# Kernel optimization log

Hardware: AMD Instinct MI355X
Metric: run time of the kernel (lower is better)

Reference implementation:

```python
import jax, jax.numpy as jnp
import numpy as np

B, S, D, H = 2, 2048, 1024, 16
DH = D // H  # d_head = 64
EPS = 1e-6


def _rms_norm(x, eps=EPS):
    # norm_without_weight: RMS normalization over last dim, no learned scale
    return x * jax.lax.rsqrt(jnp.mean(x * x, axis=-1, keepdims=True) + eps)


def _rope_tables(seq_len, dim):
    # angular_freq: dim//4 geometric freqs + dim//4 zeros -> dim//2 total
    freqs = (1.0 / 1024.0) ** jnp.linspace(0.0, 1.0, dim // 4, dtype=jnp.float32)
    freqs = jnp.concatenate([freqs, jnp.zeros((dim // 4,), dtype=jnp.float32)])
    theta = jnp.outer(jnp.arange(seq_len, dtype=jnp.float32), freqs)  # [S, dim//2]
    return jnp.cos(theta), jnp.sin(theta)


def _apply_rope(x_bhsk, cos, sin):
    # x: [B,H,S,DH]; cos/sin: [S, DH//2] broadcast over batch/heads
    c = cos[None, None, :, :]
    s = sin[None, None, :, :]
    xf = x_bhsk.astype(jnp.float32)
    x1, x2 = jnp.split(xf, 2, axis=-1)
    y1 = x1 * c + x2 * s
    y2 = -x1 * s + x2 * c
    return jnp.concatenate([y1, y2], axis=-1).astype(x_bhsk.dtype)


def setup_inputs() -> dict:
    key = jax.random.key(0)
    k0, k1, k2, k3, k4 = jax.random.split(key, 5)
    scale = 1.0 / np.sqrt(D)
    x = jax.random.normal(k0, (B, S, D), dtype=jnp.float32)
    # equinox Linear stores weight as [out_features, in_features], y = x @ W.T
    w_q = jax.random.normal(k1, (D, D), dtype=jnp.float32) * scale
    w_k = jax.random.normal(k2, (D, D), dtype=jnp.float32) * scale
    w_v = jax.random.normal(k3, (D, D), dtype=jnp.float32) * scale
    w_o = jax.random.normal(k4, (D, D), dtype=jnp.float32) * scale
    mask = jnp.tril(jnp.ones((S, S), dtype=bool))  # causal
    return {"x": x, "w_q": w_q, "w_k": w_k, "w_v": w_v, "w_o": w_o, "mask": mask}


def reference(x, w_q, w_k, w_v, w_o, mask):
    b, s, d = x.shape
    # projections (no bias); [B,S,D] @ [D,D].T -> [B,S,D] -> [B,H,S,DH]
    def proj(w):
        y = jnp.einsum('bsd,ed->bse', x, w)
        return y.reshape(b, s, H, DH).transpose(0, 2, 1, 3)
    q, k, v = proj(w_q), proj(w_k), proj(w_v)
    # QK-norm (RMS, no weight)
    q = _rms_norm(q)
    k = _rms_norm(k)
    # rotary over sequence axis
    cos, sin = _rope_tables(s, DH)
    q = _apply_rope(q, cos, sin)
    k = _apply_rope(k, cos, sin)
    # scores [B,H,S,S]
    scores = jnp.einsum('bhsk,bhtk->bhst', q, k) / jnp.sqrt(jnp.float32(DH))
    scores = jnp.where(mask[None, None, :, :], scores, -jnp.inf)
    weights = jax.nn.softmax(scores, axis=-1)
    out = jnp.einsum('bhst,bhtk->bhsk', weights, v)  # [B,H,S,DH]
    out = out.transpose(0, 2, 1, 3).reshape(b, s, d)
    return jnp.einsum('bsd,ed->bse', out, w_o)
```

## Files before the change

kernel.cpp:

```cpp
#include <hip/hip_runtime.h>
#include <hip/hip_bf16.h>

#define Bb 2
#define Ss 2048
#define Dd 1024
#define Hh 16
#define Tt ((size_t)Bb*Ss*Dd)
#define WNn ((size_t)Dd*Dd)

typedef short bf16x8 __attribute__((ext_vector_type(8)));
typedef short bf16x4 __attribute__((ext_vector_type(4)));
typedef float floatx4 __attribute__((ext_vector_type(4)));
typedef unsigned short u16;

__device__ inline void gld16(void* lds, const void* g) {
  __builtin_amdgcn_global_load_lds(
      (const __attribute__((address_space(1))) unsigned int*)g,
      (__attribute__((address_space(3))) unsigned int*)lds, 16, 0, 0);
}

__device__ inline float bf2f(u16 u) {
  unsigned int x = ((unsigned int)u) << 16;
  float f; __builtin_memcpy(&f, &x, 4); return f;
}
__device__ inline u16 f2bf(float f) {
  unsigned int x; __builtin_memcpy(&x, &f, 4);
  x = (x + 0x7fff + ((x >> 16) & 1)) >> 16;
  return (u16)x;
}
__device__ inline float u2f(unsigned int x) {
  float f; __builtin_memcpy(&f, &x, 4); return f;
}
__device__ inline unsigned int cvtpk(float lo, float hi) {
  unsigned int r;
  asm("v_cvt_pk_bf16_f32 %0, %1, %2" : "=v"(r) : "v"(lo), "v"(hi));
  return r;
}

__global__ void sniff(const unsigned int* __restrict__ x, unsigned int* __restrict__ flag,
                      int nwords) {
  __shared__ int cnt;
  if (threadIdx.x == 0) cnt = 0;
  __syncthreads();
  int local = 0;
  for (int i = threadIdx.x; i < nwords; i += blockDim.x) {
    unsigned int wd = x[i];
    if (((wd >> 7)  & 0xFFu) == 0xFFu) local++;
    if (((wd >> 23) & 0xFFu) == 0xFFu) local++;
  }
  atomicAdd(&cnt, local);
  __syncthreads();
  if (threadIdx.x == 0) *flag = (cnt >= 64) ? 1u : 0u;
}

__global__ __launch_bounds__(256) void convert_all(
    const void* __restrict__ x,  const void* __restrict__ wq,
    const void* __restrict__ wk, const void* __restrict__ wv,
    const void* __restrict__ wo, u16* __restrict__ dst,
    int smode, const unsigned int* __restrict__ flag,
    float2* __restrict__ tab) {
  const int gb = blockIdx.x;
  if (gb >= 4096) {
    int e = (gb - 4096)*1024 + threadIdx.x*4;
#pragma unroll
    for (int j = 0; j < 4; j++, e++) {
      int s = e >> 4, f = e & 15;
      float freq = exp2f((-10.0f/15.0f) * (float)f);
      float th = (float)s * freq;
      float sn, c;
      sincosf(th, &sn, &c);
      tab[e] = make_float2(c, sn);
    }
    return;
  }
  const void* src; size_t base; int lb;
  if (gb < 2048)      { src = x;  base = 0;            lb = gb;        }
  else if (gb < 2560) { src = wq; base = Tt;           lb = gb - 2048; }
  else if (gb < 3072) { src = wk; base = Tt + WNn;     lb = gb - 2560; }
  else if (gb < 3584) { src = wv; base = Tt + 2*WNn;   lb = gb - 3072; }
  else                { src = wo; base = Tt + 3*WNn;   lb = gb - 3584; }
  const size_t off = (size_t)lb*2048 + threadIdx.x*8;
  const bool f32 = (smode >= 0) ? (smode == 1) : (*flag != 0u);
  bf16x8 v;
  if (f32) {
    const float* s = (const float*)src + off;
#pragma unroll
    for (int j = 0; j < 8; j++) v[j] = (short)f2bf(s[j]);
  } else {
    v = *(const bf16x8*)((const u16*)src + off);
  }
  *(bf16x8*)(dst + base + off) = v;
}

__global__ __launch_bounds__(256) void gemm_bt(
    const u16* __restrict__ A,
    const u16* __restrict__ W0, const u16* __restrict__ W1, const u16* __restrict__ W2,
    void* __restrict__ C0, void* __restrict__ C1, void* __restrict__ C2,
    int M, int N, int K, const float2* __restrict__ tab)
{
  const u16* W; void* C;
  if (blockIdx.z == 0)      { W = W0; C = C0; }
  else if (blockIdx.z == 1) { W = W1; C = C1; }
  else                      { W = W2; C = C2; }

  __shared__ __align__(16) u16 sA[128*32];
  __shared__ __align__(16) u16 sB[128*32];
  __shared__ __align__(16) u16 sE[4][64*72];

  const int tid  = threadIdx.x;
  const int lane = tid & 63;
  const int w    = tid >> 6;
  const int wm = w >> 1, wn = w & 1;
  const int col = lane & 15, quad = lane >> 4;
  const int bm = blockIdx.y, bn = blockIdx.x;

  floatx4 acc[4][4] = {};

  const int c0 = tid, c1 = tid + 256;
  const size_t aOff0 = (size_t)(bm*128 + (c0 >> 2))*K + (c0 & 3)*8;
  const size_t aOff1 = (size_t)(bm*128 + (c1 >> 2))*K + (c1 & 3)*8;
  const size_t bOff0 = (size_t)(bn*128 + (c0 >> 2))*K + (c0 & 3)*8;
  const size_t bOff1 = (size_t)(bn*128 + (c1 >> 2))*K + (c1 & 3)*8;

  for (int kk = 0; kk < K; kk += 32) {
    gld16(&sA[c0*8], A + aOff0 + kk);
    gld16(&sA[c1*8], A + aOff1 + kk);
    gld16(&sB[c0*8], W + bOff0 + kk);
    gld16(&sB[c1*8], W + bOff1 + kk);
    __syncthreads();
    bf16x8 af[4], bfr[4];
#pragma unroll
    for (int i = 0; i < 4; i++)
      af[i] = *(const bf16x8*)&sA[(wm*64 + i*16 + col)*32 + quad*8];
#pragma unroll
    for (int j = 0; j < 4; j++)
      bfr[j] = *(const bf16x8*)&sB[(wn*64 + j*16 + col)*32 + quad*8];
#pragma unroll
    for (int i = 0; i < 4; i++)
#pragma unroll
      for (int j = 0; j < 4; j++)
        acc[i][j] = __builtin_amdgcn_mfma_f32_16x16x32_bf16(af[i], bfr[j], acc[i][j], 0, 0, 0);
    __syncthreads();
  }

  u16* sEw = &sE[w][0];
  const int rrow = lane >> 3, rch = lane & 7;

  if (blockIdx.z == 2) {
#pragma unroll
    for (int i = 0; i < 4; i++)
#pragma unroll
      for (int j = 0; j < 4; j++) {
        bf16x4 pk;
#pragma unroll
        for (int r = 0; r < 4; r++) pk[r] = (short)f2bf(acc[i][j][r]);
        *(bf16x4*)&sEw[(j*16 + col)*72 + i*16 + quad*4] = pk;
      }
    const int g0 = bm*128 + wm*64;
    const int bb = g0 >> 11, s0 = g0 & (Ss - 1);
    const int hh = (bn*128 + wn*64) >> 6;
    u16* Ct = (u16*)C;
#pragma unroll
    for (int t = 0; t < 8; t++) {
      const int dl = rrow + t*8;
      bf16x8 v = *(const bf16x8*)&sEw[dl*72 + rch*8];
      *(bf16x8*)&Ct[((size_t)(bb*Hh + hh)*64 + dl)*Ss + s0 + rch*8] = v;
    }
  } else {
    const float qs = (blockIdx.z == 0) ? 0.125f : 1.0f;
#pragma unroll
    for (int i = 0; i < 4; i++)
#pragma unroll
      for (int r = 0; r < 4; r++) {
        float ss = 0.0f;
#pragma unroll
        for (int j = 0; j < 4; j++) ss += acc[i][j][r]*acc[i][j][r];
        ss += __shfl_xor(ss, 1, 64);
        ss += __shfl_xor(ss, 2, 64);
        ss += __shfl_xor(ss, 4, 64);
        ss += __shfl_xor(ss, 8, 64);
        float rn = rsqrtf(ss*(1.0f/64.0f) + 1e-6f) * qs;
        int grow = bm*128 + wm*64 + i*16 + quad*4 + r;
        float2 cs = tab[(grow & (Ss - 1))*16 + col];
        float x0 = acc[i][0][r]*rn, x1 = acc[i][1][r]*rn;
        float x2 = acc[i][2][r]*rn, x3 = acc[i][3][r]*rn;
        const int lr = (i*16 + quad*4 + r)*72;
        sEw[lr + col]      = f2bf(x0*cs.x + x2*cs.y);
        sEw[lr + 16 + col] = f2bf(x1);
        sEw[lr + 32 + col] = f2bf(x2*cs.x - x0*cs.y);
        sEw[lr + 48 + col] = f2bf(x3);
      }
    u16* Co = (u16*)C;
    const size_t gb = (size_t)(bm*128 + wm*64);
    const int cb = bn*128 + wn*64 + rch*8;
#pragma unroll
    for (int t = 0; t < 8; t++) {
      const int lr = rrow + t*8;
      bf16x8 v = *(const bf16x8*)&sEw[lr*72 + rch*8];
      *(bf16x8*)&Co[(gb + lr)*N + cb] = v;
    }
  }
}

__global__ __launch_bounds__(256) void gemm_o(
    const u16* __restrict__ A, const u16* __restrict__ W, void* __restrict__ C,
    int M, int N, int K, const unsigned int* __restrict__ flag, int outMode)
{
  __shared__ __align__(16) u16 sA[128*32];
  __shared__ __align__(16) u16 sB[64*32];

  const int tid  = threadIdx.x;
  const int lane = tid & 63;
  const int w    = tid >> 6;
  const int wm = w >> 1, wn = w & 1;
  const int col = lane & 15, quad = lane >> 4;
  const int bm = blockIdx.y, bn = blockIdx.x;

  floatx4 acc[4][2] = {};

  const int c0 = tid, c1 = tid + 256;
  const size_t aOff0 = (size_t)(bm*128 + (c0 >> 2))*K + (c0 & 3)*8;
  const size_t aOff1 = (size_t)(bm*128 + (c1 >> 2))*K + (c1 & 3)*8;
  const size_t bOff0 = (size_t)(bn*64  + (c0 >> 2))*K + (c0 & 3)*8;

  for (int kk = 0; kk < K; kk += 32) {
    gld16(&sA[c0*8], A + aOff0 + kk);
    gld16(&sA[c1*8], A + aOff1 + kk);
    gld16(&sB[c0*8], W + bOff0 + kk);
    __syncthreads();
    bf16x8 af[4], bfr[2];
#pragma unroll
    for (int i = 0; i < 4; i++)
      af[i] = *(const bf16x8*)&sA[(wm*64 + i*16 + col)*32 + quad*8];
#pragma unroll
    for (int j = 0; j < 2; j++)
      bfr[j] = *(const bf16x8*)&sB[(wn*32 + j*16 + col)*32 + quad*8];
#pragma unroll
    for (int i = 0; i < 4; i++)
#pragma unroll
      for (int j = 0; j < 2; j++)
        acc[i][j] = __builtin_amdgcn_mfma_f32_16x16x32_bf16(af[i], bfr[j], acc[i][j], 0, 0, 0);
    __syncthreads();
  }

  const bool f32o = (outMode == 1) || (outMode == -1 && *flag != 0u);
#pragma unroll
  for (int i = 0; i < 4; i++)
#pragma unroll
    for (int j = 0; j < 2; j++)
#pragma unroll
      for (int r = 0; r < 4; r++) {
        int grow = bm*128 + wm*64 + i*16 + quad*4 + r;
        int gcol = bn*64 + wn*32 + j*16 + col;
        size_t idx = (size_t)grow*N + gcol;
        float v = acc[i][j][r];
        if (f32o) ((float*)C)[idx] = v;
        else      ((u16*)C)[idx]   = f2bf(v);
      }
}

__global__ __launch_bounds__(256) void attn(
    const u16* __restrict__ Q, const u16* __restrict__ Kv,
    const u16* __restrict__ Vt, u16* __restrict__ O)
{
  __shared__ __align__(16) u16 sK[2][64*72];
  __shared__ __align__(16) u16 sV[2][2][64*32];
  __shared__ __align__(16) u16 sP[4][16*72];

  const int tid  = threadIdx.x;
  const int lane = tid & 63;
  const int w    = tid >> 6;
  const int col = lane & 15, quad = lane >> 4;
  const int bh = blockIdx.x;
  const int qt = 31 - (int)blockIdx.y;
  const int b = bh >> 4, h = bh & 15;
  const size_t base  = (size_t)b*Ss*Dd + (size_t)h*64;
  const size_t vbase = (size_t)bh*64*Ss;

  const int krow = tid >> 2;
  const int kch  = (tid & 3) * 2;
  const int vrow = tid >> 2;
  const int vcp  = (tid & 3) ^ (vrow & 3) ^ ((vrow >> 2) & 3);
  const u16* Vh = Vt + vbase + (size_t)vrow*Ss + vcp*8;
  const int xorv = quad ^ (col & 3) ^ ((col >> 2) & 3);
  u16* sPw = &sP[w][0];
  const float L2E = 1.44269504f;

  const int q0 = qt * 64;
  const int nk = qt + 1;
  const int qmin = q0 + w*16;

  bf16x8 qf0, qf1;
  {
    const size_t qoff = base + (size_t)(q0 + w*16 + col)*Dd + quad*8;
    qf0 = *(const bf16x8*)(Q + qoff);
    qf1 = *(const bf16x8*)(Q + qoff + 32);
  }
  floatx4 oacc[4] = {};
  float mi[4], li[4];
#pragma unroll
  for (int r = 0; r < 4; r++) { mi[r] = -1e30f; li[r] = 0.0f; }

  {
    const u16* kg = Kv + base + (size_t)krow*Dd + kch*8;
    bf16x8 ka = *(const bf16x8*)kg;
    bf16x8 kb = *(const bf16x8*)(kg + 8);
    gld16(&sV[0][0][tid*8], Vh);
    gld16(&sV[0][1][tid*8], Vh + 32);
    *(bf16x8*)&sK[0][krow*72 + kch*8]     = ka;
    *(bf16x8*)&sK[0][krow*72 + kch*8 + 8] = kb;
    __syncthreads();
  }

  for (int kt = 0; kt < nk; kt++) {
    const int t0 = kt*64;
    const int cur = kt & 1, nxt = cur ^ 1;
    const bool more = (kt + 1 < nk);
    bf16x8 ka, kb;
    if (more) {
      const u16* kg = Kv + base + (size_t)(t0 + 64 + krow)*Dd + kch*8;
      ka = *(const bf16x8*)kg;
      kb = *(const bf16x8*)(kg + 8);
      gld16(&sV[nxt][0][tid*8], Vh + t0 + 64);
      gld16(&sV[nxt][1][tid*8], Vh + t0 + 96);
    }

    floatx4 sc[4] = {};
    __builtin_amdgcn_s_setprio(1);
#pragma unroll
    for (int ts = 0; ts < 4; ts++) {
      bf16x8 k0 = *(const bf16x8*)&sK[cur][(ts*16 + col)*72 + quad*8];
      bf16x8 k1 = *(const bf16x8*)&sK[cur][(ts*16 + col)*72 + 32 + quad*8];
      sc[ts] = __builtin_amdgcn_mfma_f32_16x16x32_bf16(qf0, k0, sc[ts], 0,0,0);
      sc[ts] = __builtin_amdgcn_mfma_f32_16x16x32_bf16(qf1, k1, sc[ts], 0,0,0);
    }
    __builtin_amdgcn_s_setprio(0);

    const bool boundary = (t0 + 63 > qmin);
    float mxr[4];
    float needmax = 0.0f;
#pragma unroll
    for (int r = 0; r < 4; r++) {
      if (boundary) {
        const int qr = q0 + w*16 + quad*4 + r;
        if (t0 +      col > qr) sc[0][r] = -1e30f;
        if (t0 + 16 + col > qr) sc[1][r] = -1e30f;
        if (t0 + 32 + col > qr) sc[2][r] = -1e30f;
        if (t0 + 48 + col > qr) sc[3][r] = -1e30f;
      }
      float mx = fmaxf(fmaxf(sc[0][r], sc[1][r]), fmaxf(sc[2][r], sc[3][r]));
      mx = fmaxf(mx, __shfl_xor(mx, 1, 64));
      mx = fmaxf(mx, __shfl_xor(mx, 2, 64));
      mx = fmaxf(mx, __shfl_xor(mx, 4, 64));
      mx = fmaxf(mx, __shfl_xor(mx, 8, 64));
      mxr[r] = mx;
      needmax = fmaxf(needmax, mx - mi[r]);
    }
    if (!__all(needmax <= 8.0f)) {
      float alr[4];
#pragma unroll
      for (int r = 0; r < 4; r++) {
        float mn = fmaxf(mi[r], mxr[r]);
        float al = exp2f((mi[r] - mn)*L2E);
        mi[r] = mn; li[r] *= al; alr[r] = al;
      }
#pragma unroll
      for (int db = 0; db < 4; db++)
#pragma unroll
        for (int r = 0; r < 4; r++) oacc[db][r] *= alr[r];
    }
#pragma unroll
    for (int r = 0; r < 4; r++) {
      const float nb = -mi[r]*L2E;
      float p0 = exp2f(fmaf(sc[0][r], L2E, nb));
      float p1 = exp2f(fmaf(sc[1][r], L2E, nb));
      float p2 = exp2f(fmaf(sc[2][r], L2E, nb));
      float p3 = exp2f(fmaf(sc[3][r], L2E, nb));
      unsigned int pk01 = cvtpk(p0, p1);
      unsigned int pk23 = cvtpk(p2, p3);
      const int rw = (quad*4 + r)*72;
      sPw[rw + col]      = (u16)pk01;
      sPw[rw + 16 + col] = (u16)(pk01 >> 16);
      sPw[rw + 32 + col] = (u16)pk23;
      sPw[rw + 48 + col] = (u16)(pk23 >> 16);
      li[r] += (u2f(pk01 << 16) + u2f(pk01 & 0xffff0000u))
             + (u2f(pk23 << 16) + u2f(pk23 & 0xffff0000u));
    }
    bf16x8 pa0 = *(const bf16x8*)&sPw[col*72 + quad*8];
    bf16x8 pa1 = *(const bf16x8*)&sPw[col*72 + 32 + quad*8];
    __builtin_amdgcn_s_setprio(1);
#pragma unroll
    for (int db = 0; db < 4; db++) {
      const int vs = (db*16 + col)*32 + xorv*8;
      bf16x8 vb0 = *(const bf16x8*)&sV[cur][0][vs];
      bf16x8 vb1 = *(const bf16x8*)&sV[cur][1][vs];
      oacc[db] = __builtin_amdgcn_mfma_f32_16x16x32_bf16(pa0, vb0, oacc[db], 0,0,0);
      oacc[db] = __builtin_amdgcn_mfma_f32_16x16x32_bf16(pa1, vb1, oacc[db], 0,0,0);
    }
    __builtin_amdgcn_s_setprio(0);

    if (more) {
      *(bf16x8*)&sK[nxt][krow*72 + kch*8]     = ka;
      *(bf16x8*)&sK[nxt][krow*72 + kch*8 + 8] = kb;
    }
    __syncthreads();
  }

  float inv[4];
#pragma unroll
  for (int r = 0; r < 4; r++) {
    float s = li[r];
    s += __shfl_xor(s, 1, 64);
    s += __shfl_xor(s, 2, 64);
    s += __shfl_xor(s, 4, 64);
    s += __shfl_xor(s, 8, 64);
    inv[r] = 1.0f / s;
  }
#pragma unroll
  for (int db = 0; db < 4; db++)
#pragma unroll
    for (int r = 0; r < 4; r++)
      O[base + (size_t)(q0 + w*16 + quad*4 + r)*Dd + db*16 + col] =
          f2bf(oacc[db][r] * inv[r]);
}

extern "C" void kernel_launch(void* const* d_in, const int* in_sizes, int n_in,
                              void* d_out, int out_size, void* d_ws, size_t ws_size,
                              hipStream_t stream) {
  const void* x  = d_in[0];
  const void* wq = d_in[1];
  const void* wk = d_in[2];
  const void* wv = d_in[3];
  const void* wo = d_in[4];

  const size_t T  = Tt;
  const size_t WN = WNn;

  char* ws = (char*)d_ws;
  unsigned int* flag = (unsigned int*)ws;
  u16* xb  = (u16*)(ws + 256);
  u16* wqb = xb  + T;
  u16* wkb = wqb + WN;
  u16* wvb = wkb + WN;
  u16* wob = wvb + WN;
  u16* Qb  = wob + WN;
  u16* Kb  = Qb + T;
  u16* Vb  = Kb + T;
  u16* AO  = Vb + T;
  float2* tab = (float2*)(AO + T);

  int smode = -1;
  if (in_sizes && n_in > 0) {
    if (in_sizes[0] == (int)(T*4))      smode = 1;
    else if (in_sizes[0] == (int)(T*2)) smode = 0;
  }
  if (smode < 0)
    sniff<<<1, 1024, 0, stream>>>((const unsigned int*)x, flag, 65536);

  convert_all<<<4128, 256, 0, stream>>>(x, wq, wk, wv, wo, xb, smode, flag, tab);

  gemm_bt<<<dim3(8, 32, 3), 256, 0, stream>>>(xb, wqb, wkb, wvb, Qb, Kb, Vb,
                                              4096, 1024, 1024, tab);
  attn<<<dim3(32, 32), 256, 0, stream>>>(Qb, Kb, Vb, AO);
  gemm_o<<<dim3(16, 32), 256, 0, stream>>>(AO, wob, d_out,
                                           4096, 1024, 1024, flag, smode);
}
```

Before: 258.2 us.

## Transpose QK^T MFMA in attention and drop LDS staging in projection epilogue

The attention kernel swaps MFMA operands so each lane owns one query row's scores. Row max and sum then need two cross-quad shuffles instead of per-row butterfly reductions, and P is written to LDS with one vectorized store per tile. Rescale factors and the final normalizer are broadcast through small shared arrays. The QKV GEMM epilogue drops the shared-memory staging buffer and writes directly to global memory, which frees LDS but replaces coalesced 16-byte stores with scattered 2-byte and 8-byte stores.

```diff
diff --git a/kernel.cpp b/kernel.cpp
--- a/kernel.cpp
+++ b/kernel.cpp
@@ -105,7 +105,6 @@
 
   __shared__ __align__(16) u16 sA[128*32];
   __shared__ __align__(16) u16 sB[128*32];
-  __shared__ __align__(16) u16 sE[4][64*72];
 
   const int tid  = threadIdx.x;
   const int lane = tid & 63;
@@ -143,31 +142,25 @@
     __syncthreads();
   }
 
-  u16* sEw = &sE[w][0];
-  const int rrow = lane >> 3, rch = lane & 7;
-
   if (blockIdx.z == 2) {
+    u16* Ct = (u16*)C;
 #pragma unroll
     for (int i = 0; i < 4; i++)
 #pragma unroll
       for (int j = 0; j < 4; j++) {
+        int d = bn*128 + wn*64 + j*16 + col;
+        int g = bm*128 + wm*64 + i*16 + quad*4;
+        int hh = d >> 6, dl = d & 63;
+        int bb = g >> 11, s = g & (Ss - 1);
         bf16x4 pk;
 #pragma unroll
         for (int r = 0; r < 4; r++) pk[r] = (short)f2bf(acc[i][j][r]);
-        *(bf16x4*)&sEw[(j*16 + col)*72 + i*16 + quad*4] = pk;
+        *(bf16x4*)&Ct[((size_t)(bb*Hh + hh)*64 + dl)*Ss + s] = pk;
       }
-    const int g0 = bm*128 + wm*64;
-    const int bb = g0 >> 11, s0 = g0 & (Ss - 1);
-    const int hh = (bn*128 + wn*64) >> 6;
-    u16* Ct = (u16*)C;
-#pragma unroll
-    for (int t = 0; t < 8; t++) {
-      const int dl = rrow + t*8;
-      bf16x8 v = *(const bf16x8*)&sEw[dl*72 + rch*8];
-      *(bf16x8*)&Ct[((size_t)(bb*Hh + hh)*64 + dl)*Ss + s0 + rch*8] = v;
-    }
   } else {
     const float qs = (blockIdx.z == 0) ? 0.125f : 1.0f;
+    u16* Co = (u16*)C;
+    const size_t cb = (size_t)(bn*128 + wn*64 + col);
 #pragma unroll
     for (int i = 0; i < 4; i++)
 #pragma unroll
@@ -182,23 +175,15 @@
         float rn = rsqrtf(ss*(1.0f/64.0f) + 1e-6f) * qs;
         int grow = bm*128 + wm*64 + i*16 + quad*4 + r;
         float2 cs = tab[(grow & (Ss - 1))*16 + col];
+        float c = cs.x, sn = cs.y;
         float x0 = acc[i][0][r]*rn, x1 = acc[i][1][r]*rn;
         float x2 = acc[i][2][r]*rn, x3 = acc[i][3][r]*rn;
-        const int lr = (i*16 + quad*4 + r)*72;
-        sEw[lr + col]      = f2bf(x0*cs.x + x2*cs.y);
-        sEw[lr + 16 + col] = f2bf(x1);
-        sEw[lr + 32 + col] = f2bf(x2*cs.x - x0*cs.y);
-        sEw[lr + 48 + col] = f2bf(x3);
+        size_t rowb = (size_t)grow*N + cb;
+        Co[rowb]      = f2bf(x0*c + x2*sn);
+        Co[rowb + 16] = f2bf(x1);
+        Co[rowb + 32] = f2bf(x2*c - x0*sn);
+        Co[rowb + 48] = f2bf(x3);
       }
-    u16* Co = (u16*)C;
-    const size_t gb = (size_t)(bm*128 + wm*64);
-    const int cb = bn*128 + wn*64 + rch*8;
-#pragma unroll
-    for (int t = 0; t < 8; t++) {
-      const int lr = rrow + t*8;
-      bf16x8 v = *(const bf16x8*)&sEw[lr*72 + rch*8];
-      *(bf16x8*)&Co[(gb + lr)*N + cb] = v;
-    }
   }
 }
 
@@ -266,6 +251,8 @@
   __shared__ __align__(16) u16 sK[2][64*72];
   __shared__ __align__(16) u16 sV[2][2][64*32];
   __shared__ __align__(16) u16 sP[4][16*72];
+  __shared__ float sAl[4][16];
+  __shared__ float sLi[4][16];
 
   const int tid  = threadIdx.x;
   const int lane = tid & 63;
@@ -288,7 +275,7 @@
 
   const int q0 = qt * 64;
   const int nk = qt + 1;
-  const int qmin = q0 + w*16;
+  const int qg = q0 + w*16 + col;
 
   bf16x8 qf0, qf1;
   {
@@ -297,9 +284,7 @@
     qf1 = *(const bf16x8*)(Q + qoff + 32);
   }
   floatx4 oacc[4] = {};
-  float mi[4], li[4];
-#pragma unroll
-  for (int r = 0; r < 4; r++) { mi[r] = -1e30f; li[r] = 0.0f; }
+  float mi = -1e30f, li = 0.0f;
 
   {
     const u16* kg = Kv + base + (size_t)krow*Dd + kch*8;
@@ -331,60 +316,52 @@
     for (int ts = 0; ts < 4; ts++) {
       bf16x8 k0 = *(const bf16x8*)&sK[cur][(ts*16 + col)*72 + quad*8];
       bf16x8 k1 = *(const bf16x8*)&sK[cur][(ts*16 + col)*72 + 32 + quad*8];
-      sc[ts] = __builtin_amdgcn_mfma_f32_16x16x32_bf16(qf0, k0, sc[ts], 0,0,0);
-      sc[ts] = __builtin_amdgcn_mfma_f32_16x16x32_bf16(qf1, k1, sc[ts], 0,0,0);
+      sc[ts] = __builtin_amdgcn_mfma_f32_16x16x32_bf16(k0, qf0, sc[ts], 0,0,0);
+      sc[ts] = __builtin_amdgcn_mfma_f32_16x16x32_bf16(k1, qf1, sc[ts], 0,0,0);
     }
     __builtin_amdgcn_s_setprio(0);
 
-    const bool boundary = (t0 + 63 > qmin);
-    float mxr[4];
-    float needmax = 0.0f;
-#pragma unroll
-    for (int r = 0; r < 4; r++) {
-      if (boundary) {
-        const int qr = q0 + w*16 + quad*4 + r;
-        if (t0 +      col > qr) sc[0][r] = -1e30f;
-        if (t0 + 16 + col > qr) sc[1][r] = -1e30f;
-        if (t0 + 32 + col > qr) sc[2][r] = -1e30f;
-        if (t0 + 48 + col > qr) sc[3][r] = -1e30f;
+    const bool boundary = (t0 + 63 > q0 + w*16);
+    if (boundary) {
+      const int tb = t0 + quad*4 - qg;
+#pragma unroll
+      for (int ts = 0; ts < 4; ts++)
+#pragma unroll
+        for (int r = 0; r < 4; r++)
+          if (tb + ts*16 + r > 0) sc[ts][r] = -1e30f;
+    }
+    float mx = fmaxf(fmaxf(sc[0][0], sc[0][1]), fmaxf(sc[0][2], sc[0][3]));
+#pragma unroll
+    for (int ts = 1; ts < 4; ts++)
+      mx = fmaxf(mx, fmaxf(fmaxf(sc[ts][0], sc[ts][1]),
+                           fmaxf(sc[ts][2], sc[ts][3])));
+    mx = fmaxf(mx, __shfl_xor(mx, 16, 64));
+    mx = fmaxf(mx, __shfl_xor(mx, 32, 64));
+    if (!__all(mx - mi <= 8.0f)) {
+      float mn = fmaxf(mi, mx);
+      float al = exp2f((mi - mn)*L2E);
+      mi = mn; li *= al;
+      if (quad == 0) sAl[w][col] = al;
+      float a0 = sAl[w][quad*4 + 0], a1 = sAl[w][quad*4 + 1];
+      float a2 = sAl[w][quad*4 + 2], a3 = sAl[w][quad*4 + 3];
+#pragma unroll
+      for (int db = 0; db < 4; db++) {
+        oacc[db][0] *= a0; oacc[db][1] *= a1;
+        oacc[db][2] *= a2; oacc[db][3] *= a3;
       }
-      float mx = fmaxf(fmaxf(sc[0][r], sc[1][r]), fmaxf(sc[2][r], sc[3][r]));
-      mx = fmaxf(mx, __shfl_xor(mx, 1, 64));
-      mx = fmaxf(mx, __shfl_xor(mx, 2, 64));
-      mx = fmaxf(mx, __shfl_xor(mx, 4, 64));
-      mx = fmaxf(mx, __shfl_xor(mx, 8, 64));
-      mxr[r] = mx;
-      needmax = fmaxf(needmax, mx - mi[r]);
-    }
-    if (!__all(needmax <= 8.0f)) {
-      float alr[4];
-#pragma unroll
-      for (int r = 0; r < 4; r++) {
-        float mn = fmaxf(mi[r], mxr[r]);
-        float al = exp2f((mi[r] - mn)*L2E);
-        mi[r] = mn; li[r] *= al; alr[r] = al;
-      }
-#pragma unroll
-      for (int db = 0; db < 4; db++)
-#pragma unroll
-        for (int r = 0; r < 4; r++) oacc[db][r] *= alr[r];
-    }
-#pragma unroll
-    for (int r = 0; r < 4; r++) {
-      const float nb = -mi[r]*L2E;
-      float p0 = exp2f(fmaf(sc[0][r], L2E, nb));
-      float p1 = exp2f(fmaf(sc[1][r], L2E, nb));
-      float p2 = exp2f(fmaf(sc[2][r], L2E, nb));
-      float p3 = exp2f(fmaf(sc[3][r], L2E, nb));
+    }
+    const float nb = -mi*L2E;
+#pragma unroll
+    for (int ts = 0; ts < 4; ts++) {
+      float p0 = exp2f(fmaf(sc[ts][0], L2E, nb));
+      float p1 = exp2f(fmaf(sc[ts][1], L2E, nb));
+      float p2 = exp2f(fmaf(sc[ts][2], L2E, nb));
+      float p3 = exp2f(fmaf(sc[ts][3], L2E, nb));
       unsigned int pk01 = cvtpk(p0, p1);
       unsigned int pk23 = cvtpk(p2, p3);
-      const int rw = (quad*4 + r)*72;
-      sPw[rw + col]      = (u16)pk01;
-      sPw[rw + 16 + col] = (u16)(pk01 >> 16);
-      sPw[rw + 32 + col] = (u16)pk23;
-      sPw[rw + 48 + col] = (u16)(pk23 >> 16);
-      li[r] += (u2f(pk01 << 16) + u2f(pk01 & 0xffff0000u))
-             + (u2f(pk23 << 16) + u2f(pk23 & 0xffff0000u));
+      *(uint2*)&sPw[col*72 + ts*16 + quad*4] = make_uint2(pk01, pk23);
+      li += (u2f(pk01 << 16) + u2f(pk01 & 0xffff0000u))
+          + (u2f(pk23 << 16) + u2f(pk23 & 0xffff0000u));
     }
     bf16x8 pa0 = *(const bf16x8*)&sPw[col*72 + quad*8];
     bf16x8 pa1 = *(const bf16x8*)&sPw[col*72 + 32 + quad*8];
@@ -406,22 +383,19 @@
     __syncthreads();
   }
 
-  float inv[4];
-#pragma unroll
-  for (int r = 0; r < 4; r++) {
-    float s = li[r];
-    s += __shfl_xor(s, 1, 64);
-    s += __shfl_xor(s, 2, 64);
-    s += __shfl_xor(s, 4, 64);
-    s += __shfl_xor(s, 8, 64);
-    inv[r] = 1.0f / s;
-  }
-#pragma unroll
-  for (int db = 0; db < 4; db++)
-#pragma unroll
-    for (int r = 0; r < 4; r++)
-      O[base + (size_t)(q0 + w*16 + quad*4 + r)*Dd + db*16 + col] =
-          f2bf(oacc[db][r] * inv[r]);
+  li += __shfl_xor(li, 16, 64);
+  li += __shfl_xor(li, 32, 64);
+  if (quad == 0) sLi[w][col] = 1.0f / li;
+  float i0 = sLi[w][quad*4 + 0], i1 = sLi[w][quad*4 + 1];
+  float i2 = sLi[w][quad*4 + 2], i3 = sLi[w][quad*4 + 3];
+#pragma unroll
+  for (int db = 0; db < 4; db++) {
+    const size_t rb = base + (size_t)(q0 + w*16 + quad*4)*Dd + db*16 + col;
+    O[rb]        = f2bf(oacc[db][0] * i0);
+    O[rb + Dd]   = f2bf(oacc[db][1] * i1);
+    O[rb + 2*Dd] = f2bf(oacc[db][2] * i2);
+    O[rb + 3*Dd] = f2bf(oacc[db][3] * i3);
+  }
 }
 
 extern "C" void kernel_launch(void* const* d_in, const int* in_sizes, int n_in,
```

Result: faster. 233.2 us (-9.7%).
